# Performance work log

Hardware: AMD Instinct MI355X
Metric: run time of the kernel (lower is better)

## Reference

```python
import jax, jax.numpy as jnp
import numpy as np

N, F, E = 50000, 128, 800000
H, C1, C2 = 4, 32, 32  # heads, channel_in, channel_out
LRELU_SLOPE = 0.2
LN_EPS = 1e-5


def _gat_conv(x, src, dst, W_src, W_dst, att_src, att_dst, bias, n, h, c):
    # x: [n, f_in]; src/dst: [e] edge endpoints (message j->i)
    xs = (x @ W_src).reshape(n, h, c)  # source-side transform
    xd = (x @ W_dst).reshape(n, h, c)  # dest-side transform
    a_s = jnp.einsum('nhc,hc->nh', xs, att_src)  # [n,h]
    a_d = jnp.einsum('nhc,hc->nh', xd, att_dst)
    e = jax.nn.leaky_relu(a_s[src] + a_d[dst], LRELU_SLOPE)  # [E,h]
    m = jax.lax.stop_gradient(jax.ops.segment_max(e, dst, num_segments=n))
    ee = jnp.exp(e - m[dst])
    denom = jax.ops.segment_sum(ee, dst, num_segments=n)
    alpha = ee / (denom[dst] + 1e-16)  # segment softmax over incoming edges
    out = jax.ops.segment_sum(xs[src] * alpha[:, :, None], dst, num_segments=n)
    return out.reshape(n, h * c) + bias


def _layer_norm(x, gamma, beta):
    mu = jnp.mean(x, axis=-1, keepdims=True)
    var = jnp.var(x, axis=-1, keepdims=True)
    return (x - mu) * jax.lax.rsqrt(var + LN_EPS) * gamma + beta


def setup_inputs() -> dict:
    key = jax.random.key(0)
    ks = jax.random.split(key, 16)
    hid = H * C1  # 128
    out_dim = H * C2  # 128

    def glorot(k, shape, fan_in):
        return jax.random.normal(k, shape, dtype=jnp.float32) / np.sqrt(fan_in)

    x = jax.random.normal(ks[0], (N, F), dtype=jnp.float32)
    edge_index = jax.random.randint(ks[1], (2, E), 0, N, dtype=jnp.int32)

    return {
        'x': x,
        'edge_index': edge_index,
        # conv1 (in F -> H*C1)
        'W1_src': glorot(ks[2], (F, H * C1), F),
        'W1_dst': glorot(ks[3], (F, H * C1), F),
        'att1_src': glorot(ks[4], (H, C1), C1),
        'att1_dst': glorot(ks[5], (H, C1), C1),
        'b1': jnp.zeros((H * C1,), jnp.float32),
        # lin1 skip (F -> hid)
        'Wl1': glorot(ks[6], (F, hid), F),
        'bl1': jnp.zeros((hid,), jnp.float32),
        # LayerNorm over hid
        'gamma': jnp.ones((hid,), jnp.float32),
        'beta': jnp.zeros((hid,), jnp.float32),
        # conv2 (hid -> H*C2)
        'W2_src': glorot(ks[7], (hid, H * C2), hid),
        'W2_dst': glorot(ks[8], (hid, H * C2), hid),
        'att2_src': glorot(ks[9], (H, C2), C2),
        'att2_dst': glorot(ks[10], (H, C2), C2),
        'b2': jnp.zeros((H * C2,), jnp.float32),
        # lin2 skip (hid -> out_dim)
        'Wl2': glorot(ks[11], (hid, out_dim), hid),
        'bl2': jnp.zeros((out_dim,), jnp.float32),
    }


def reference(x, edge_index, W1_src, W1_dst, att1_src, att1_dst, b1, Wl1, bl1,
              gamma, beta, W2_src, W2_dst, att2_src, att2_dst, b2, Wl2, bl2):
    src, dst = edge_index[0], edge_index[1]
    h = _gat_conv(x, src, dst, W1_src, W1_dst, att1_src, att1_dst, b1, N, H, C1) \
        + (x @ Wl1 + bl1)
    h = jax.nn.relu(_layer_norm(h, gamma, beta))
    out = _gat_conv(h, src, dst, W2_src, W2_dst, att2_src, att2_dst, b2, N, H, C2) \
        + (h @ Wl2 + bl2)
    return out
```

## Files before the change

kernel.cpp:

```cpp
#include <hip/hip_runtime.h>

#define N_NODES 50000
#define E_EDGES 800000
#define LRELU 0.2f
#define LN_EPS 1e-5f
#define NBUCK 98
#define BSHIFT 9

typedef short bf16x8 __attribute__((ext_vector_type(8)));
typedef float f32x4 __attribute__((ext_vector_type(4)));

__device__ __forceinline__ ushort f2bf(float f) {
    uint u = __float_as_uint(f);
    u += 0x7FFF + ((u >> 16) & 1);
    return (ushort)(u >> 16);
}
__device__ __forceinline__ float bflo(uint u) { return __uint_as_float(u << 16); }
__device__ __forceinline__ float bfhi(uint u) { return __uint_as_float(u & 0xFFFF0000u); }

__global__ __launch_bounds__(256) void bucket_count_kernel(
    const int* __restrict__ dst, int* __restrict__ bucketCnt, int e)
{
    __shared__ int lhist[NBUCK];
    int t = threadIdx.x;
    if (t < NBUCK) lhist[t] = 0;
    __syncthreads();
    int e0 = blockIdx.x * 2048;
    int count = min(2048, e - e0);
    #pragma unroll
    for (int q = 0; q < 8; ++q) {
        int li = t + q * 256;
        if (li < count) atomicAdd(&lhist[dst[e0 + li] >> BSHIFT], 1);
    }
    __syncthreads();
    if (t < NBUCK && lhist[t]) atomicAdd(&bucketCnt[t], lhist[t]);
}

__global__ __launch_bounds__(128) void bucket_scan_kernel(
    const int* __restrict__ bucketCnt, int* __restrict__ bucketBase,
    int* __restrict__ bucketCursor)
{
    __shared__ int ls[128];
    int t = threadIdx.x;
    int v = (t < NBUCK) ? bucketCnt[t] : 0;
    ls[t] = v;
    __syncthreads();
    #pragma unroll
    for (int off = 1; off < 128; off <<= 1) {
        int u = (t >= off) ? ls[t - off] : 0;
        __syncthreads();
        ls[t] += u;
        __syncthreads();
    }
    if (t < NBUCK) {
        int ex = ls[t] - v;
        bucketBase[t] = ex;
        bucketCursor[t] = ex;
    }
    if (t == NBUCK - 1) bucketBase[NBUCK] = ls[t];
}

__global__ __launch_bounds__(256) void bucket_scatter_kernel(
    const int* __restrict__ src, const int* __restrict__ dst,
    int* __restrict__ bucketCursor, uint* __restrict__ pairs, int e)
{
    __shared__ int lhist[128];
    __shared__ int lscan[NBUCK];
    __shared__ int lcur[NBUCK];
    __shared__ int lbase[NBUCK];
    __shared__ uint stageW[2048];
    __shared__ int  stageA[2048];
    int t = threadIdx.x;
    int e0 = blockIdx.x * 2048;
    int count = min(2048, e - e0);

    if (t < 128) lhist[t] = 0;
    if (t < NBUCK) lcur[t] = 0;
    __syncthreads();

    int  bb[8];
    uint pk[8];
    #pragma unroll
    for (int q = 0; q < 8; ++q) {
        int li = t + q * 256;
        if (li < count) {
            int d = dst[e0 + li];
            int s = src[e0 + li];
            bb[q] = d >> BSHIFT;
            pk[q] = (uint)s | ((uint)(d & 511) << 16);
            atomicAdd(&lhist[bb[q]], 1);
        } else bb[q] = -1;
    }
    __syncthreads();

    int orig = (t < 128) ? lhist[t] : 0;
    #pragma unroll
    for (int off = 1; off < 128; off <<= 1) {
        int u = 0;
        if (t < 128 && t >= off) u = lhist[t - off];
        __syncthreads();
        if (t < 128) lhist[t] += u;
        __syncthreads();
    }
    if (t < NBUCK) {
        lscan[t] = lhist[t] - orig;
        lbase[t] = orig ? atomicAdd(&bucketCursor[t], orig) : 0;
    }
    __syncthreads();

    #pragma unroll
    for (int q = 0; q < 8; ++q) {
        if (bb[q] >= 0) {
            int slot = lscan[bb[q]] + atomicAdd(&lcur[bb[q]], 1);
            stageW[slot] = pk[q];
            stageA[slot] = lbase[bb[q]] + (slot - lscan[bb[q]]);
        }
    }
    __syncthreads();

    #pragma unroll
    for (int q = 0; q < 8; ++q) {
        int li = t + q * 256;
        if (li < count) pairs[stageA[li]] = stageW[li];
    }
}

__global__ __launch_bounds__(512) void bucket_sort_kernel(
    const uint* __restrict__ pairs, const int* __restrict__ bucketBase,
    int* __restrict__ offs, ushort* __restrict__ srcSorted, int n, int e)
{
    __shared__ int cnt[512], cur[512], ls[512];
    int b = blockIdx.x, t = threadIdx.x;
    int base = bucketBase[b];
    int m = bucketBase[b + 1] - base;
    cnt[t] = 0; cur[t] = 0;
    __syncthreads();
    for (int i = t; i < m; i += 512)
        atomicAdd(&cnt[pairs[base + i] >> 16], 1);
    __syncthreads();
    int orig = cnt[t];
    ls[t] = orig;
    __syncthreads();
    #pragma unroll
    for (int off = 1; off < 512; off <<= 1) {
        int u = (t >= off) ? ls[t - off] : 0;
        __syncthreads();
        ls[t] += u;
        __syncthreads();
    }
    int excl = ls[t] - orig;
    int node = (b << BSHIFT) + t;
    if (node < n) offs[node] = base + excl;
    if (b == NBUCK - 1 && t == 0) offs[n] = e;
    cnt[t] = excl;
    __syncthreads();
    for (int i = t; i < m; i += 512) {
        uint w = pairs[base + i];
        int dl = w >> 16;
        int pos = cnt[dl] + atomicAdd(&cur[dl], 1);
        srcSorted[base + pos] = (ushort)(w & 0xFFFFu);
    }
}

__global__ __launch_bounds__(256) void prep_all_kernel(
    const float* __restrict__ W1s, const float* __restrict__ Wl1,
    const float* __restrict__ W1d, const float* __restrict__ a1s,
    const float* __restrict__ a1d,
    const float* __restrict__ W2s, const float* __restrict__ Wl2,
    const float* __restrict__ W2d, const float* __restrict__ a2s,
    const float* __restrict__ a2d,
    ushort* __restrict__ Wt, ushort* __restrict__ Watt)
{
    int t = threadIdx.x;
    if (blockIdx.x < 256) {
        int idx = blockIdx.x * 256 + t;
        int lw = idx >> 14, rem = idx & 16383;
        int nn = rem >> 7, k = rem & 127;
        const float* W = (lw == 0) ? W1s : (lw == 1) ? Wl1 : (lw == 2) ? W2s : Wl2;
        Wt[idx] = f2bf(W[k * 128 + nn]);
    } else {
        int L = blockIdx.x - 256;
        const float* Ws = L ? W2s : W1s;
        const float* Wd = L ? W2d : W1d;
        const float* as = L ? a2s : a1s;
        const float* adv = L ? a2d : a1d;
        #pragma unroll
        for (int q = 0; q < 8; ++q) {
            int e = q * 256 + t;
            int c = e >> 7, f = e & 127;
            float v = 0.f;
            if (c < 8) {
                const float* W  = (c < 4) ? Ws : Wd;
                const float* av = (c < 4) ? as : adv;
                int h = c & 3;
                #pragma unroll
                for (int j = 0; j < 32; ++j)
                    v += W[f * 128 + h * 32 + j] * av[h * 32 + j];
            }
            Watt[L * 2048 + c * 128 + f] = f2bf(v);
        }
    }
}

template <int LAYER>
__global__ __launch_bounds__(256) void gemm_fused_kernel(
    const float* __restrict__ Afp, const ushort* __restrict__ Abf,
    const ushort* __restrict__ Wt, const ushort* __restrict__ Watt,
    ushort* __restrict__ Cbf, float* __restrict__ a_sd, int n)
{
    __shared__ ushort Asb[64][136];
    __shared__ ushort Wsb[128][136];
    __shared__ ushort Attb[16][136];
    const int z = blockIdx.x;
    const int row0 = blockIdx.y * 64;
    const int tid = threadIdx.x;

    if (LAYER == 0) {
        #pragma unroll
        for (int i = 0; i < 8; ++i) {
            int idx = tid + i * 256;
            int r = idx >> 5, c4 = idx & 31;
            int grow = row0 + r;
            float4 v = make_float4(0.f, 0.f, 0.f, 0.f);
            if (grow < n) v = *(const float4*)(Afp + (size_t)grow * 128 + c4 * 4);
            ushort4 o;
            o.x = f2bf(v.x); o.y = f2bf(v.y); o.z = f2bf(v.z); o.w = f2bf(v.w);
            *(ushort4*)&Asb[r][c4 * 4] = o;
        }
    } else {
        #pragma unroll
        for (int i = 0; i < 4; ++i) {
            int c = tid + i * 256;
            int r = c >> 4, o = c & 15;
            int grow = row0 + r;
            uint4 v = make_uint4(0, 0, 0, 0);
            if (grow < n) v = *(const uint4*)(Abf + (size_t)grow * 128 + o * 8);
            *(uint4*)&Asb[r][o * 8] = v;
        }
    }
    {
        const ushort* Wz = Wt + (size_t)(LAYER * 2 + z) * 16384;
        #pragma unroll
        for (int i = 0; i < 8; ++i) {
            int c = tid + i * 256;
            int r = c >> 4, o = c & 15;
            uint4 v = *(const uint4*)(Wz + r * 128 + o * 8);
            *(uint4*)&Wsb[r][o * 8] = v;
        }
    }
    if (z == 0) {
        int r = tid >> 4, o = tid & 15;
        uint4 v = *(const uint4*)(Watt + LAYER * 2048 + r * 128 + o * 8);
        *(uint4*)&Attb[r][o * 8] = v;
    }
    __syncthreads();

    const int w = tid >> 6, lane = tid & 63;
    const int wm = w >> 1, wn = w & 1;
    const int l15 = lane & 15, lg = lane >> 4;
    const bool doAtt = (z == 0) && (wn == 0);

    f32x4 acc[2][4];
    f32x4 accA[2];
    #pragma unroll
    for (int m = 0; m < 2; ++m) {
        accA[m] = (f32x4){0.f, 0.f, 0.f, 0.f};
        #pragma unroll
        for (int j = 0; j < 4; ++j)
            acc[m][j] = (f32x4){0.f, 0.f, 0.f, 0.f};
    }

    #pragma unroll
    for (int ks = 0; ks < 4; ++ks) {
        const int k0 = ks * 32 + 4 * lg;
        bf16x8 af[2], bfr[4];
        #pragma unroll
        for (int m = 0; m < 2; ++m) {
            const ushort* p = &Asb[wm * 32 + m * 16 + l15][k0];
            ushort4 lo = *(const ushort4*)p;
            ushort4 hi = *(const ushort4*)(p + 16);
            bf16x8 a;
            a[0] = (short)lo.x; a[1] = (short)lo.y; a[2] = (short)lo.z; a[3] = (short)lo.w;
            a[4] = (short)hi.x; a[5] = (short)hi.y; a[6] = (short)hi.z; a[7] = (short)hi.w;
            af[m] = a;
        }
        #pragma unroll
        for (int j = 0; j < 4; ++j) {
            const ushort* p = &Wsb[wn * 64 + j * 16 + l15][k0];
            ushort4 lo = *(const ushort4*)p;
            ushort4 hi = *(const ushort4*)(p + 16);
            bf16x8 b;
            b[0] = (short)lo.x; b[1] = (short)lo.y; b[2] = (short)lo.z; b[3] = (short)lo.w;
            b[4] = (short)hi.x; b[5] = (short)hi.y; b[6] = (short)hi.z; b[7] = (short)hi.w;
            bfr[j] = b;
        }
        #pragma unroll
        for (int m = 0; m < 2; ++m)
            #pragma unroll
            for (int j = 0; j < 4; ++j)
                acc[m][j] = __builtin_amdgcn_mfma_f32_16x16x32_bf16(
                    af[m], bfr[j], acc[m][j], 0, 0, 0);
        if (doAtt) {
            const ushort* p = &Attb[l15][k0];
            ushort4 lo = *(const ushort4*)p;
            ushort4 hi = *(const ushort4*)(p + 16);
            bf16x8 b;
            b[0] = (short)lo.x; b[1] = (short)lo.y; b[2] = (short)lo.z; b[3] = (short)lo.w;
            b[4] = (short)hi.x; b[5] = (short)hi.y; b[6] = (short)hi.z; b[7] = (short)hi.w;
            #pragma unroll
            for (int m = 0; m < 2; ++m)
                accA[m] = __builtin_amdgcn_mfma_f32_16x16x32_bf16(
                    af[m], b, accA[m], 0, 0, 0);
        }
    }

    #pragma unroll
    for (int m = 0; m < 2; ++m)
        #pragma unroll
        for (int j = 0; j < 4; ++j)
            #pragma unroll
            for (int r = 0; r < 4; ++r) {
                int grow = row0 + wm * 32 + m * 16 + lg * 4 + r;
                if (grow < n)
                    Cbf[(size_t)grow * 256 + z * 128 + wn * 64 + j * 16 + l15] =
                        f2bf(acc[m][j][r]);
            }
    if (doAtt && l15 < 8) {
        #pragma unroll
        for (int m = 0; m < 2; ++m)
            #pragma unroll
            for (int r = 0; r < 4; ++r) {
                int grow = row0 + wm * 32 + m * 16 + lg * 4 + r;
                if (grow < n) a_sd[(size_t)grow * 8 + l15] = accA[m][r];
            }
    }
}

template <int MODE>
__global__ __launch_bounds__(256) void aggregate_fused_kernel(
    const ushort* __restrict__ srcSorted, const int* __restrict__ offs,
    const ushort* __restrict__ bufbf,
    const float* __restrict__ a_sd,
    const float* __restrict__ bias_a, const float* __restrict__ bias_l,
    const float* __restrict__ gamma, const float* __restrict__ beta,
    ushort* __restrict__ hbf, float* __restrict__ out, int n)
{
    int node = (blockIdx.x * blockDim.x + threadIdx.x) >> 6;
    int lane = threadIdx.x & 63;
    if (node >= n) return;
    int beg = offs[node], end = offs[node + 1];
    int h = lane >> 4;
    float ad = a_sd[(size_t)node * 8 + 4 + h];
    int hh = (lane >> 3) & 3;
    float adh = __shfl(ad, hh << 4);
    int j8 = lane & 7;
    int h8 = (lane >> 4) << 3;

    float num0 = 0.f, num1 = 0.f, den = 0.f;
    int t = beg;
    int nb = (end - beg) >> 3;

    for (int b = 0; b < nb; ++b, t += 8) {
        int s = 0; float ee = 0.f;
        if (lane < 32) {
            s = srcSorted[t + j8];
            float as = a_sd[(size_t)s * 8 + hh];
            float e = as + adh;
            e = (e > 0.f) ? e : LRELU * e;
            ee = __expf(e);
        }
        #pragma unroll
        for (int q = 0; q < 8; ++q) {
            float eeq = __shfl(ee, h8 + q);
            int   sq  = __shfl(s, q);
            uint xq = *(const uint*)(bufbf + (size_t)sq * 256 + 2 * lane);
            num0 += eeq * bflo(xq);
            num1 += eeq * bfhi(xq);
            den  += eeq;
        }
    }
    for (; t < end; ++t) {
        int s0 = srcSorted[t];
        float as0 = a_sd[(size_t)s0 * 8 + h];
        uint x0 = *(const uint*)(bufbf + (size_t)s0 * 256 + 2 * lane);
        float e0 = as0 + ad;
        e0 = (e0 > 0.f) ? e0 : LRELU * e0;
        float ee0 = __expf(e0);
        num0 += ee0 * bflo(x0);
        num1 += ee0 * bfhi(x0);
        den  += ee0;
    }

    float inv = 1.f / (den + 1e-16f);
    uint sk = *(const uint*)(bufbf + (size_t)node * 256 + 128 + 2 * lane);
    float2 ba = *(const float2*)(bias_a + 2 * lane);
    float2 bl = *(const float2*)(bias_l + 2 * lane);
    float v0 = num0 * inv + bflo(sk) + ba.x + bl.x;
    float v1 = num1 * inv + bfhi(sk) + ba.y + bl.y;

    if (MODE == 0) {
        float sum = v0 + v1, sq = v0 * v0 + v1 * v1;
        #pragma unroll
        for (int off = 32; off; off >>= 1) {
            sum += __shfl_xor(sum, off);
            sq  += __shfl_xor(sq, off);
        }
        float mu = sum * (1.f / 128.f);
        float var = sq * (1.f / 128.f) - mu * mu;
        float rs = rsqrtf(var + LN_EPS);
        float2 gm = *(const float2*)(gamma + 2 * lane);
        float2 bt = *(const float2*)(beta + 2 * lane);
        float o0 = fmaxf((v0 - mu) * rs * gm.x + bt.x, 0.f);
        float o1 = fmaxf((v1 - mu) * rs * gm.y + bt.y, 0.f);
        uint packed = (uint)f2bf(o0) | ((uint)f2bf(o1) << 16);
        *(uint*)(hbf + (size_t)node * 128 + 2 * lane) = packed;
    } else {
        *(float2*)(out + (size_t)node * 128 + 2 * lane) = make_float2(v0, v1);
    }
}

extern "C" void kernel_launch(void* const* d_in, const int* in_sizes, int n_in,
                              void* d_out, int out_size, void* d_ws, size_t ws_size,
                              hipStream_t stream) {
    const float* x       = (const float*)d_in[0];
    const int*   ei      = (const int*)d_in[1];
    const int*   src     = ei;
    const int*   dst     = ei + E_EDGES;
    const float* W1_src  = (const float*)d_in[2];
    const float* W1_dst  = (const float*)d_in[3];
    const float* att1_s  = (const float*)d_in[4];
    const float* att1_d  = (const float*)d_in[5];
    const float* b1      = (const float*)d_in[6];
    const float* Wl1     = (const float*)d_in[7];
    const float* bl1     = (const float*)d_in[8];
    const float* gamma   = (const float*)d_in[9];
    const float* beta    = (const float*)d_in[10];
    const float* W2_src  = (const float*)d_in[11];
    const float* W2_dst  = (const float*)d_in[12];
    const float* att2_s  = (const float*)d_in[13];
    const float* att2_d  = (const float*)d_in[14];
    const float* b2      = (const float*)d_in[15];
    const float* Wl2     = (const float*)d_in[16];
    const float* bl2     = (const float*)d_in[17];
    float* out = (float*)d_out;

    char* p = (char*)d_ws;
    float* a_sd        = (float*)p;      p += (size_t)N_NODES * 8 * 4;
    int* offs          = (int*)p;        p += (size_t)(N_NODES + 1) * 4;
    int* bucketCnt     = (int*)p;        p += (NBUCK) * 4;
    int* bucketBase    = (int*)p;        p += (NBUCK + 1) * 4;
    int* bucketCursor  = (int*)p;        p += (NBUCK + 1) * 4;
    uint* pairs        = (uint*)p;       p += (size_t)E_EDGES * 4;
    ushort* hbf        = (ushort*)p;     p += (size_t)N_NODES * 128 * 2;
    ushort* bufbf      = (ushort*)p;     p += (size_t)N_NODES * 256 * 2;
    ushort* Wt         = (ushort*)p;     p += (size_t)4 * 16384 * 2;
    ushort* Watt       = (ushort*)p;     p += (size_t)2 * 2048 * 2;
    ushort* srcSorted  = (ushort*)p;     p += (size_t)E_EDGES * 2;

    dim3 ggrid(2, (N_NODES + 63) / 64);
    int edge_blocks = (E_EDGES + 2047) / 2048;
    int wave_grid   = (N_NODES + 3) / 4;

    hipMemsetAsync(bucketCnt, 0, NBUCK * sizeof(int), stream);
    bucket_count_kernel<<<edge_blocks, 256, 0, stream>>>(dst, bucketCnt, E_EDGES);
    bucket_scan_kernel<<<1, 128, 0, stream>>>(bucketCnt, bucketBase, bucketCursor);
    bucket_scatter_kernel<<<edge_blocks, 256, 0, stream>>>(src, dst, bucketCursor, pairs, E_EDGES);
    bucket_sort_kernel<<<NBUCK, 512, 0, stream>>>(pairs, bucketBase, offs, srcSorted, N_NODES, E_EDGES);

    prep_all_kernel<<<258, 256, 0, stream>>>(
        W1_src, Wl1, W1_dst, att1_s, att1_d,
        W2_src, Wl2, W2_dst, att2_s, att2_d, Wt, Watt);

    gemm_fused_kernel<0><<<ggrid, 256, 0, stream>>>(x, nullptr, Wt, Watt, bufbf, a_sd, N_NODES);
    aggregate_fused_kernel<0><<<wave_grid, 256, 0, stream>>>(
        srcSorted, offs, bufbf, a_sd, b1, bl1, gamma, beta, hbf, nullptr, N_NODES);

    gemm_fused_kernel<1><<<ggrid, 256, 0, stream>>>(nullptr, hbf, Wt, Watt, bufbf, a_sd, N_NODES);
    aggregate_fused_kernel<1><<<wave_grid, 256, 0, stream>>>(
        srcSorted, offs, bufbf, a_sd, b2, bl2, nullptr, nullptr, nullptr, out, N_NODES);
}
```

Before: 322.1 us.

## Aggregate four edges per wavefront step with 16-byte gathers per lane

The per-node aggregation kernel now splits the 64-lane wavefront into four groups of 16 lanes. Each group handles a different incoming edge and loads 16 bytes (8 bf16 features) per lane instead of 4 bytes. Partial sums are combined across groups with xor shuffles, and the bias, skip, LayerNorm and output steps run on 16 lanes with vectorized loads and stores. The goal is more independent gathers in flight and fewer, wider memory transactions per edge. In exchange, tail edges are padded by clamping the index, which wastes lanes on low-degree nodes, and 48 lanes sit idle during the epilogue.

```diff
diff --git a/kernel.cpp b/kernel.cpp
--- a/kernel.cpp
+++ b/kernel.cpp
@@ -349,73 +349,104 @@
     int lane = threadIdx.x & 63;
     if (node >= n) return;
     int beg = offs[node], end = offs[node + 1];
-    int h = lane >> 4;
-    float ad = a_sd[(size_t)node * 8 + 4 + h];
-    int hh = (lane >> 3) & 3;
-    float adh = __shfl(ad, hh << 4);
-    int j8 = lane & 7;
-    int h8 = (lane >> 4) << 3;
-
-    float num0 = 0.f, num1 = 0.f, den = 0.f;
-    int t = beg;
-    int nb = (end - beg) >> 3;
-
-    for (int b = 0; b < nb; ++b, t += 8) {
+    const int j = lane >> 4;
+    const int g = lane & 15;
+    const int h = g >> 2;
+    const int je = lane & 3, he = lane >> 2;
+
+    float adh = 0.f;
+    if (lane < 16) adh = a_sd[(size_t)node * 8 + 4 + he];
+
+    float acc[8] = {};
+    float denp = 0.f;
+
+    for (int t = beg; t < end; t += 4) {
         int s = 0; float ee = 0.f;
-        if (lane < 32) {
-            s = srcSorted[t + j8];
-            float as = a_sd[(size_t)s * 8 + hh];
+        if (lane < 16) {
+            int idx = t + je;
+            int ic = (idx < end) ? idx : (end - 1);
+            s = srcSorted[ic];
+            float as = a_sd[(size_t)s * 8 + he];
             float e = as + adh;
             e = (e > 0.f) ? e : LRELU * e;
-            ee = __expf(e);
-        }
-        #pragma unroll
-        for (int q = 0; q < 8; ++q) {
-            float eeq = __shfl(ee, h8 + q);
-            int   sq  = __shfl(s, q);
-            uint xq = *(const uint*)(bufbf + (size_t)sq * 256 + 2 * lane);
-            num0 += eeq * bflo(xq);
-            num1 += eeq * bfhi(xq);
-            den  += eeq;
-        }
-    }
-    for (; t < end; ++t) {
-        int s0 = srcSorted[t];
-        float as0 = a_sd[(size_t)s0 * 8 + h];
-        uint x0 = *(const uint*)(bufbf + (size_t)s0 * 256 + 2 * lane);
-        float e0 = as0 + ad;
-        e0 = (e0 > 0.f) ? e0 : LRELU * e0;
-        float ee0 = __expf(e0);
-        num0 += ee0 * bflo(x0);
-        num1 += ee0 * bfhi(x0);
-        den  += ee0;
-    }
-
-    float inv = 1.f / (den + 1e-16f);
-    uint sk = *(const uint*)(bufbf + (size_t)node * 256 + 128 + 2 * lane);
-    float2 ba = *(const float2*)(bias_a + 2 * lane);
-    float2 bl = *(const float2*)(bias_l + 2 * lane);
-    float v0 = num0 * inv + bflo(sk) + ba.x + bl.x;
-    float v1 = num1 * inv + bfhi(sk) + ba.y + bl.y;
-
-    if (MODE == 0) {
-        float sum = v0 + v1, sq = v0 * v0 + v1 * v1;
-        #pragma unroll
-        for (int off = 32; off; off >>= 1) {
-            sum += __shfl_xor(sum, off);
-            sq  += __shfl_xor(sq, off);
-        }
-        float mu = sum * (1.f / 128.f);
-        float var = sq * (1.f / 128.f) - mu * mu;
-        float rs = rsqrtf(var + LN_EPS);
-        float2 gm = *(const float2*)(gamma + 2 * lane);
-        float2 bt = *(const float2*)(beta + 2 * lane);
-        float o0 = fmaxf((v0 - mu) * rs * gm.x + bt.x, 0.f);
-        float o1 = fmaxf((v1 - mu) * rs * gm.y + bt.y, 0.f);
-        uint packed = (uint)f2bf(o0) | ((uint)f2bf(o1) << 16);
-        *(uint*)(hbf + (size_t)node * 128 + 2 * lane) = packed;
-    } else {
-        *(float2*)(out + (size_t)node * 128 + 2 * lane) = make_float2(v0, v1);
+            ee = (idx < end) ? __expf(e) : 0.f;
+            denp += ee;
+        }
+        int   sq  = __shfl(s, j);
+        float eeq = __shfl(ee, h * 4 + j);
+        uint4 xv = *(const uint4*)(bufbf + (size_t)sq * 256 + g * 8);
+        acc[0] = fmaf(eeq, bflo(xv.x), acc[0]);
+        acc[1] = fmaf(eeq, bfhi(xv.x), acc[1]);
+        acc[2] = fmaf(eeq, bflo(xv.y), acc[2]);
+        acc[3] = fmaf(eeq, bfhi(xv.y), acc[3]);
+        acc[4] = fmaf(eeq, bflo(xv.z), acc[4]);
+        acc[5] = fmaf(eeq, bfhi(xv.z), acc[5]);
+        acc[6] = fmaf(eeq, bflo(xv.w), acc[6]);
+        acc[7] = fmaf(eeq, bfhi(xv.w), acc[7]);
+    }
+
+    #pragma unroll
+    for (int c = 0; c < 8; ++c) {
+        acc[c] += __shfl_xor(acc[c], 16);
+        acc[c] += __shfl_xor(acc[c], 32);
+    }
+    denp += __shfl_xor(denp, 1);
+    denp += __shfl_xor(denp, 2);
+
+    if (lane < 16) {
+        float inv = 1.f / (denp + 1e-16f);
+        uint4 sk = *(const uint4*)(bufbf + (size_t)node * 256 + 128 + g * 8);
+        float4 ba0 = *(const float4*)(bias_a + g * 8);
+        float4 ba1 = *(const float4*)(bias_a + g * 8 + 4);
+        float4 bl0 = *(const float4*)(bias_l + g * 8);
+        float4 bl1 = *(const float4*)(bias_l + g * 8 + 4);
+        float v[8];
+        v[0] = acc[0] * inv + bflo(sk.x) + ba0.x + bl0.x;
+        v[1] = acc[1] * inv + bfhi(sk.x) + ba0.y + bl0.y;
+        v[2] = acc[2] * inv + bflo(sk.y) + ba0.z + bl0.z;
+        v[3] = acc[3] * inv + bfhi(sk.y) + ba0.w + bl0.w;
+        v[4] = acc[4] * inv + bflo(sk.z) + ba1.x + bl1.x;
+        v[5] = acc[5] * inv + bfhi(sk.z) + ba1.y + bl1.y;
+        v[6] = acc[6] * inv + bflo(sk.w) + ba1.z + bl1.z;
+        v[7] = acc[7] * inv + bfhi(sk.w) + ba1.w + bl1.w;
+
+        if (MODE == 0) {
+            float sum = 0.f, sq = 0.f;
+            #pragma unroll
+            for (int c = 0; c < 8; ++c) { sum += v[c]; sq += v[c] * v[c]; }
+            #pragma unroll
+            for (int off = 1; off < 16; off <<= 1) {
+                sum += __shfl_xor(sum, off);
+                sq  += __shfl_xor(sq, off);
+            }
+            float mu = sum * (1.f / 128.f);
+            float var = sq * (1.f / 128.f) - mu * mu;
+            float rs = rsqrtf(var + LN_EPS);
+            float4 gm0 = *(const float4*)(gamma + g * 8);
+            float4 gm1 = *(const float4*)(gamma + g * 8 + 4);
+            float4 bt0 = *(const float4*)(beta + g * 8);
+            float4 bt1 = *(const float4*)(beta + g * 8 + 4);
+            float o[8];
+            o[0] = fmaxf((v[0] - mu) * rs * gm0.x + bt0.x, 0.f);
+            o[1] = fmaxf((v[1] - mu) * rs * gm0.y + bt0.y, 0.f);
+            o[2] = fmaxf((v[2] - mu) * rs * gm0.z + bt0.z, 0.f);
+            o[3] = fmaxf((v[3] - mu) * rs * gm0.w + bt0.w, 0.f);
+            o[4] = fmaxf((v[4] - mu) * rs * gm1.x + bt1.x, 0.f);
+            o[5] = fmaxf((v[5] - mu) * rs * gm1.y + bt1.y, 0.f);
+            o[6] = fmaxf((v[6] - mu) * rs * gm1.z + bt1.z, 0.f);
+            o[7] = fmaxf((v[7] - mu) * rs * gm1.w + bt1.w, 0.f);
+            uint4 st;
+            st.x = (uint)f2bf(o[0]) | ((uint)f2bf(o[1]) << 16);
+            st.y = (uint)f2bf(o[2]) | ((uint)f2bf(o[3]) << 16);
+            st.z = (uint)f2bf(o[4]) | ((uint)f2bf(o[5]) << 16);
+            st.w = (uint)f2bf(o[6]) | ((uint)f2bf(o[7]) << 16);
+            *(uint4*)(hbf + (size_t)node * 128 + g * 8) = st;
+        } else {
+            *(float4*)(out + (size_t)node * 128 + g * 8) =
+                make_float4(v[0], v[1], v[2], v[3]);
+            *(float4*)(out + (size_t)node * 128 + g * 8 + 4) =
+                make_float4(v[4], v[5], v[6], v[7]);
+        }
     }
 }
 
```

Result: no change. 325.6 us (+1.1%).
